# Performance work log

Hardware: AMD Instinct MI355X
Metric: run time of the kernel (lower is better)

## Reference

```python
import jax, jax.numpy as jnp
import numpy as np

SEQ, BS, D, F, E = 1024, 2, 2048, 2048, 8


def setup_inputs() -> dict:
    key = jax.random.key(0)
    ks = jax.random.split(key, 8)
    s = 0.02  # param init scale
    return {
        "hidden_states": jax.random.normal(ks[0], (SEQ, BS, D), jnp.float32),
        "router_w": jax.random.normal(ks[1], (D, E), jnp.float32) * s,
        "gate_w": jax.random.normal(ks[2], (E, D, F), jnp.float32) * s,
        "up_w": jax.random.normal(ks[3], (E, D, F), jnp.float32) * s,
        "down_w": jax.random.normal(ks[4], (E, F, D), jnp.float32) * s,
        "shared_gate_w": jax.random.normal(ks[5], (D, F), jnp.float32) * s,
        "shared_up_w": jax.random.normal(ks[6], (D, F), jnp.float32) * s,
        "shared_down_w": jax.random.normal(ks[7], (F, D), jnp.float32) * s,
    }


def reference(hidden_states, router_w, gate_w, up_w, down_w,
              shared_gate_w, shared_up_w, shared_down_w):
    S, B, Dm = hidden_states.shape
    x = hidden_states.reshape(-1, Dm)          # [T, D] flattened tokens
    # --- router: top-1 expert, sigmoid gate applied to the selected logit ---
    logits = x @ router_w                      # [T, E]
    expert_idx = jnp.argmax(logits, axis=-1)   # top-1 index, [T]
    score = jax.nn.sigmoid(jnp.max(logits, axis=-1))  # [T]
    xs = x * score[:, None]                    # scale BEFORE expert (Llama4)
    # --- per-expert SwiGLU MLP on masked token sets, scatter-combined ---
    n_experts = router_w.shape[1]
    out = jnp.zeros_like(x)
    for e in range(n_experts):                 # small structural loop over experts
        m = (expert_idx == e)[:, None]
        xe = jnp.where(m, xs, 0.0)             # zeroed dispatch (equiv to gather)
        h = jax.nn.silu(xe @ gate_w[e]) * (xe @ up_w[e])
        out = out + jnp.where(m, h @ down_w[e], 0.0)
    # --- shared expert on all tokens ---
    shared = (jax.nn.silu(x @ shared_gate_w) * (x @ shared_up_w)) @ shared_down_w
    return (out + shared).reshape(S, B, Dm)
```

## Files before the change

### kernel.cpp

```cpp
#include <hip/hip_runtime.h>
#include <stdint.h>
#include <math.h>

#define T_TOK 2048
#define DIM   2048
#define FDIM  2048
#define NE    8

#define BM 128
#define BN 128
#define BK 32
#define LDB 40

typedef unsigned short u16;
typedef short s16x8 __attribute__((ext_vector_type(8)));
typedef float f32x4 __attribute__((ext_vector_type(4)));

__device__ __forceinline__ u16 f2bf(float f) {
    union { float f; unsigned int u; } v; v.f = f;
    unsigned int r = v.u + 0x7FFFu + ((v.u >> 16) & 1u);
    return (u16)(r >> 16);
}

__global__ __launch_bounds__(256) void router_k(
    const float* __restrict__ x, const float* __restrict__ rw,
    float* __restrict__ score, int* __restrict__ eidx, int* __restrict__ counts)
{
    int t = blockIdx.x;
    int tid = threadIdx.x;
    float p[8] = {0.f,0.f,0.f,0.f,0.f,0.f,0.f,0.f};
    const float* xrow = x + (size_t)t * DIM;
    for (int d = tid; d < DIM; d += 256) {
        float xv = xrow[d];
        const float4* r = (const float4*)(rw + (size_t)d * 8);
        float4 r0 = r[0], r1 = r[1];
        p[0] += xv * r0.x; p[1] += xv * r0.y; p[2] += xv * r0.z; p[3] += xv * r0.w;
        p[4] += xv * r1.x; p[5] += xv * r1.y; p[6] += xv * r1.z; p[7] += xv * r1.w;
    }
    #pragma unroll
    for (int off = 32; off > 0; off >>= 1) {
        #pragma unroll
        for (int e = 0; e < 8; ++e) p[e] += __shfl_down(p[e], off);
    }
    __shared__ float red[4][8];
    int wave = tid >> 6, lane = tid & 63;
    if (lane == 0) {
        #pragma unroll
        for (int e = 0; e < 8; ++e) red[wave][e] = p[e];
    }
    __syncthreads();
    if (tid == 0) {
        float lg[8];
        #pragma unroll
        for (int e = 0; e < 8; ++e) lg[e] = red[0][e] + red[1][e] + red[2][e] + red[3][e];
        int best = 0; float bv = lg[0];
        #pragma unroll
        for (int e = 1; e < 8; ++e) { if (lg[e] > bv) { bv = lg[e]; best = e; } }
        score[t] = 1.f / (1.f + expf(-bv));
        eidx[t] = best;
        atomicAdd(&counts[best], 1);
    }
}

__global__ void scan_k(const int* __restrict__ counts, int* __restrict__ offs,
                       int* __restrict__ fill)
{
    if (threadIdx.x == 0 && blockIdx.x == 0) {
        int run = 0;
        for (int e = 0; e < NE; ++e) { offs[e] = run; fill[e] = run; run += counts[e]; }
    }
}

__global__ __launch_bounds__(256) void gather_k(
    const float* __restrict__ x, const float* __restrict__ score,
    const int* __restrict__ eidx, int* __restrict__ fill,
    int* __restrict__ tokmap, u16* __restrict__ xsc, u16* __restrict__ xbf)
{
    int t = blockIdx.x, tid = threadIdx.x;
    __shared__ int sp;
    if (tid == 0) {
        int e = eidx[t];
        int p = atomicAdd(&fill[e], 1);
        tokmap[p] = t;
        sp = p;
    }
    __syncthreads();
    int pos = sp;
    float s = score[t];
    const float4* xr = (const float4*)(x + (size_t)t * DIM);
    float4 a = xr[tid * 2], b = xr[tid * 2 + 1];
    alignas(16) u16 raw[8] = { f2bf(a.x), f2bf(a.y), f2bf(a.z), f2bf(a.w),
                               f2bf(b.x), f2bf(b.y), f2bf(b.z), f2bf(b.w) };
    alignas(16) u16 scl[8] = { f2bf(a.x*s), f2bf(a.y*s), f2bf(a.z*s), f2bf(a.w*s),
                               f2bf(b.x*s), f2bf(b.y*s), f2bf(b.z*s), f2bf(b.w*s) };
    *(s16x8*)(xbf + (size_t)t * DIM + tid * 8)   = *(s16x8*)raw;
    *(s16x8*)(xsc + (size_t)pos * DIM + tid * 8) = *(s16x8*)scl;
}

__device__ __forceinline__ void stageB(const float* __restrict__ W, u16* Bs,
                                       int bn, int bkh)
{
    const float* wp = W + (size_t)bkh * FDIM + bn;
    alignas(16) u16 tmp[16];
    #pragma unroll
    for (int j = 0; j < 16; ++j) tmp[j] = f2bf(wp[(size_t)j * FDIM]);
    *(s16x8*)&Bs[bn * LDB + bkh]     = *(s16x8*)&tmp[0];
    *(s16x8*)&Bs[bn * LDB + bkh + 8] = *(s16x8*)&tmp[8];
}

__global__ __launch_bounds__(256) void gateup_k(
    const u16* __restrict__ xsc, const u16* __restrict__ xbf,
    const float* __restrict__ gate_w, const float* __restrict__ up_w,
    const float* __restrict__ sgw, const float* __restrict__ suw,
    const int* __restrict__ counts, const int* __restrict__ offs,
    u16* __restrict__ Hbf, u16* __restrict__ Hs)
{
    int bid = blockIdx.x;
    int g  = bid >> 8;
    int mt = (bid >> 4) & 15;
    int nt = bid & 15;

    int M; const u16* A; const float* Wg; const float* Wu; u16* Ho;
    if (g < NE) {
        M = counts[g];
        int ro = offs[g];
        A  = xsc + (size_t)ro * DIM;
        Wg = gate_w + (size_t)g * DIM * FDIM;
        Wu = up_w  + (size_t)g * DIM * FDIM;
        Ho = Hbf + (size_t)ro * FDIM;
    } else {
        M = T_TOK; A = xbf; Wg = sgw; Wu = suw; Ho = Hs;
    }
    int m0 = mt * BM;
    if (m0 >= M) return;
    int n0 = nt * BN;

    __shared__ u16 As[BM * BK];
    __shared__ u16 Bg[BN * LDB];
    __shared__ u16 Bu[BN * LDB];

    int tid  = threadIdx.x;
    int lane = tid & 63;
    int wave = tid >> 6;
    int wm = (wave >> 1) * 64;
    int wn = (wave & 1) * 64;

    f32x4 accg[4][4], accu[4][4];
    #pragma unroll
    for (int i = 0; i < 4; ++i)
        #pragma unroll
        for (int j = 0; j < 4; ++j) { accg[i][j] = (f32x4)0.f; accu[i][j] = (f32x4)0.f; }

    int ar = tid >> 2;
    int ac = (tid & 3) * 8;
    int arow0 = min(m0 + ar,      M - 1);
    int arow1 = min(m0 + 64 + ar, M - 1);

    int bn  = tid & 127;
    int bkh = (tid >> 7) * 16;

    int am   = wm + (lane & 15);
    int koff = (lane >> 4) * 8;

    for (int k0 = 0; k0 < DIM; k0 += BK) {
        *(s16x8*)&As[ar * BK + ac]        = *(const s16x8*)&A[(size_t)arow0 * DIM + k0 + ac];
        *(s16x8*)&As[(64 + ar) * BK + ac] = *(const s16x8*)&A[(size_t)arow1 * DIM + k0 + ac];
        stageB(Wg + (size_t)k0 * FDIM + n0, Bg, bn, bkh);
        stageB(Wu + (size_t)k0 * FDIM + n0, Bu, bn, bkh);
        __syncthreads();

        s16x8 af[4];
        #pragma unroll
        for (int i = 0; i < 4; ++i)
            af[i] = *(const s16x8*)&As[(am + i * 16) * BK + koff];
        #pragma unroll
        for (int j = 0; j < 4; ++j) {
            int bc = wn + j * 16 + (lane & 15);
            s16x8 bg = *(const s16x8*)&Bg[bc * LDB + koff];
            s16x8 bu = *(const s16x8*)&Bu[bc * LDB + koff];
            #pragma unroll
            for (int i = 0; i < 4; ++i) {
                accg[i][j] = __builtin_amdgcn_mfma_f32_16x16x32_bf16(af[i], bg, accg[i][j], 0, 0, 0);
                accu[i][j] = __builtin_amdgcn_mfma_f32_16x16x32_bf16(af[i], bu, accu[i][j], 0, 0, 0);
            }
        }
        __syncthreads();
    }

    int rbase = wm + ((lane >> 4) << 2);
    int cbase = n0 + wn + (lane & 15);
    #pragma unroll
    for (int i = 0; i < 4; ++i) {
        #pragma unroll
        for (int j = 0; j < 4; ++j) {
            #pragma unroll
            for (int r = 0; r < 4; ++r) {
                int row = m0 + rbase + i * 16 + r;
                if (row < M) {
                    float gv = accg[i][j][r];
                    float uv = accu[i][j][r];
                    float h = gv / (1.f + expf(-gv)) * uv;
                    Ho[(size_t)row * FDIM + cbase + j * 16] = f2bf(h);
                }
            }
        }
    }
}

__global__ __launch_bounds__(256) void down_k(
    const u16* __restrict__ Hbf, const u16* __restrict__ Hs,
    const float* __restrict__ down_w, const float* __restrict__ sdw,
    const int* __restrict__ counts, const int* __restrict__ offs,
    const int* __restrict__ tokmap, float* __restrict__ out)
{
    int bid = blockIdx.x;
    int g  = bid >> 8;
    int mt = (bid >> 4) & 15;
    int nt = bid & 15;

    int M, ro; const u16* A; const float* W;
    if (g < NE) {
        M = counts[g];
        ro = offs[g];
        A = Hbf + (size_t)ro * FDIM;
        W = down_w + (size_t)g * FDIM * DIM;
    } else {
        M = T_TOK; ro = 0; A = Hs; W = sdw;
    }
    int m0 = mt * BM;
    if (m0 >= M) return;
    int n0 = nt * BN;

    __shared__ u16 As[BM * BK];
    __shared__ u16 Bd[BN * LDB];

    int tid  = threadIdx.x;
    int lane = tid & 63;
    int wave = tid >> 6;
    int wm = (wave >> 1) * 64;
    int wn = (wave & 1) * 64;

    f32x4 acc[4][4];
    #pragma unroll
    for (int i = 0; i < 4; ++i)
        #pragma unroll
        for (int j = 0; j < 4; ++j) acc[i][j] = (f32x4)0.f;

    int ar = tid >> 2;
    int ac = (tid & 3) * 8;
    int arow0 = min(m0 + ar,      M - 1);
    int arow1 = min(m0 + 64 + ar, M - 1);
    int bn  = tid & 127;
    int bkh = (tid >> 7) * 16;

    int am   = wm + (lane & 15);
    int koff = (lane >> 4) * 8;

    for (int k0 = 0; k0 < FDIM; k0 += BK) {
        *(s16x8*)&As[ar * BK + ac]        = *(const s16x8*)&A[(size_t)arow0 * FDIM + k0 + ac];
        *(s16x8*)&As[(64 + ar) * BK + ac] = *(const s16x8*)&A[(size_t)arow1 * FDIM + k0 + ac];
        stageB(W + (size_t)k0 * DIM + n0, Bd, bn, bkh);
        __syncthreads();

        s16x8 af[4];
        #pragma unroll
        for (int i = 0; i < 4; ++i)
            af[i] = *(const s16x8*)&As[(am + i * 16) * BK + koff];
        #pragma unroll
        for (int j = 0; j < 4; ++j) {
            int bc = wn + j * 16 + (lane & 15);
            s16x8 bd = *(const s16x8*)&Bd[bc * LDB + koff];
            #pragma unroll
            for (int i = 0; i < 4; ++i)
                acc[i][j] = __builtin_amdgcn_mfma_f32_16x16x32_bf16(af[i], bd, acc[i][j], 0, 0, 0);
        }
        __syncthreads();
    }

    int rbase = wm + ((lane >> 4) << 2);
    int cbase = n0 + wn + (lane & 15);
    #pragma unroll
    for (int i = 0; i < 4; ++i) {
        #pragma unroll
        for (int r = 0; r < 4; ++r) {
            int row = m0 + rbase + i * 16 + r;
            if (row < M) {
                int tok = (g < NE) ? tokmap[ro + row] : row;
                #pragma unroll
                for (int j = 0; j < 4; ++j)
                    atomicAdd(&out[(size_t)tok * DIM + cbase + j * 16], acc[i][j][r]);
            }
        }
    }
}

extern "C" void kernel_launch(void* const* d_in, const int* in_sizes, int n_in,
                              void* d_out, int out_size, void* d_ws, size_t ws_size,
                              hipStream_t stream) {
    const float* x   = (const float*)d_in[0];
    const float* rw  = (const float*)d_in[1];
    const float* gw  = (const float*)d_in[2];
    const float* uw  = (const float*)d_in[3];
    const float* dw  = (const float*)d_in[4];
    const float* sgw = (const float*)d_in[5];
    const float* suw = (const float*)d_in[6];
    const float* sdw = (const float*)d_in[7];
    float* out = (float*)d_out;

    char* ws = (char*)d_ws;
    float* score = (float*)(ws);
    int* eidx    = (int*)(ws + 8192);
    int* counts  = (int*)(ws + 16384);
    int* fill    = (int*)(ws + 16448);
    int* offs    = (int*)(ws + 16512);
    int* tokmap  = (int*)(ws + 16576);
    u16* xsc = (u16*)(ws + 32768);
    u16* xbf = (u16*)(ws + 32768 + 1ull * 8388608);
    u16* Hbf = (u16*)(ws + 32768 + 2ull * 8388608);
    u16* Hs  = (u16*)(ws + 32768 + 3ull * 8388608);

    hipMemsetAsync(counts, 0, 128, stream);
    hipMemsetAsync(out, 0, (size_t)out_size * sizeof(float), stream);

    router_k<<<T_TOK, 256, 0, stream>>>(x, rw, score, eidx, counts);
    scan_k<<<1, 64, 0, stream>>>(counts, offs, fill);
    gather_k<<<T_TOK, 256, 0, stream>>>(x, score, eidx, fill, tokmap, xsc, xbf);
    gateup_k<<<NE * 256 + 256, 256, 0, stream>>>(xsc, xbf, gw, uw, sgw, suw,
                                                 counts, offs, Hbf, Hs);
    down_k<<<NE * 256 + 256, 256, 0, stream>>>(Hbf, Hs, dw, sdw,
                                               counts, offs, tokmap, out);
}
```

Before: 792.1 us.

## Pre-convert weights to transposed bf16 and stage tiles with direct-to-LDS loads

Adds a kernel that converts all expert and shared weights from fp32 to bf16 and transposes them into K-contiguous rows in a workspace buffer each call. The GEMM kernels then load A and B tiles straight into LDS with global_load_lds 16-byte loads, in place of strided fp32 loads plus register conversion. Atomic adds in the down projection become plain stores: expert rows scatter to out and shared-expert rows go to a temp buffer that a final add kernel sums. The trade is a full pass over all 27 weight matrices every call, plus more workspace and launches, and the old path stays as a fallback when the workspace is too small.

```diff
diff --git a/kernel.cpp b/kernel.cpp
--- a/kernel.cpp
+++ b/kernel.cpp
@@ -11,6 +11,7 @@
 #define BN 128
 #define BK 32
 #define LDB 40
+#define MATSZ 4194304ull
 
 typedef unsigned short u16;
 typedef short s16x8 __attribute__((ext_vector_type(8)));
@@ -20,6 +21,11 @@
     union { float f; unsigned int u; } v; v.f = f;
     unsigned int r = v.u + 0x7FFFu + ((v.u >> 16) & 1u);
     return (u16)(r >> 16);
+}
+
+__device__ __forceinline__ void gload_lds16(const void* g, void* l) {
+    __builtin_amdgcn_global_load_lds((const __attribute__((address_space(1))) void*)g,
+                                     (__attribute__((address_space(3))) void*)l, 16, 0, 0);
 }
 
 __global__ __launch_bounds__(256) void router_k(
@@ -97,21 +103,43 @@
     *(s16x8*)(xsc + (size_t)pos * DIM + tid * 8) = *(s16x8*)scl;
 }
 
-__device__ __forceinline__ void stageB(const float* __restrict__ W, u16* Bs,
-                                       int bn, int bkh)
-{
-    const float* wp = W + (size_t)bkh * FDIM + bn;
-    alignas(16) u16 tmp[16];
-    #pragma unroll
-    for (int j = 0; j < 16; ++j) tmp[j] = f2bf(wp[(size_t)j * FDIM]);
-    *(s16x8*)&Bs[bn * LDB + bkh]     = *(s16x8*)&tmp[0];
-    *(s16x8*)&Bs[bn * LDB + bkh + 8] = *(s16x8*)&tmp[8];
+__global__ __launch_bounds__(256) void wtrans_k(
+    const float* __restrict__ gw, const float* __restrict__ uw,
+    const float* __restrict__ dwn, const float* __restrict__ sgw,
+    const float* __restrict__ suw, const float* __restrict__ sdw,
+    u16* __restrict__ wt)
+{
+    int bid = blockIdx.x;
+    int m = bid >> 5;
+    int strip = bid & 31;
+    const float* src;
+    if      (m < 8)  src = gw  + (size_t)m * MATSZ;
+    else if (m < 16) src = uw  + (size_t)(m - 8) * MATSZ;
+    else if (m < 24) src = dwn + (size_t)(m - 16) * MATSZ;
+    else if (m == 24) src = sgw;
+    else if (m == 25) src = suw;
+    else              src = sdw;
+    u16* dst = wt + (size_t)m * MATSZ;
+
+    int tid = threadIdx.x;
+    int n = strip * 64 + (tid & 63);
+    int w = tid >> 6;
+    const float* sp = src + n;
+    u16* dp = dst + (size_t)n * 2048 + w * 512;
+
+    #pragma unroll 2
+    for (int c = 0; c < 64; ++c) {
+        int k = w * 512 + c * 8;
+        alignas(16) u16 t8[8];
+        #pragma unroll
+        for (int j = 0; j < 8; ++j) t8[j] = f2bf(sp[(size_t)(k + j) * 2048]);
+        *(s16x8*)(dp + c * 8) = *(s16x8*)t8;
+    }
 }
 
 __global__ __launch_bounds__(256) void gateup_k(
     const u16* __restrict__ xsc, const u16* __restrict__ xbf,
-    const float* __restrict__ gate_w, const float* __restrict__ up_w,
-    const float* __restrict__ sgw, const float* __restrict__ suw,
+    const u16* __restrict__ wt,
     const int* __restrict__ counts, const int* __restrict__ offs,
     u16* __restrict__ Hbf, u16* __restrict__ Hs)
 {
@@ -120,30 +148,33 @@
     int mt = (bid >> 4) & 15;
     int nt = bid & 15;
 
-    int M; const u16* A; const float* Wg; const float* Wu; u16* Ho;
+    int M; const u16* A; const u16* Wg; const u16* Wu; u16* Ho;
     if (g < NE) {
         M = counts[g];
         int ro = offs[g];
         A  = xsc + (size_t)ro * DIM;
-        Wg = gate_w + (size_t)g * DIM * FDIM;
-        Wu = up_w  + (size_t)g * DIM * FDIM;
+        Wg = wt + (size_t)g * MATSZ;
+        Wu = wt + (size_t)(8 + g) * MATSZ;
         Ho = Hbf + (size_t)ro * FDIM;
     } else {
-        M = T_TOK; A = xbf; Wg = sgw; Wu = suw; Ho = Hs;
+        M = T_TOK; A = xbf;
+        Wg = wt + 24 * MATSZ;
+        Wu = wt + 25 * MATSZ;
+        Ho = Hs;
     }
     int m0 = mt * BM;
     if (m0 >= M) return;
     int n0 = nt * BN;
 
-    __shared__ u16 As[BM * BK];
-    __shared__ u16 Bg[BN * LDB];
-    __shared__ u16 Bu[BN * LDB];
+    __shared__ __align__(128) u16 As[BM * BK];
+    __shared__ __align__(128) u16 Bg[BN * BK];
+    __shared__ __align__(128) u16 Bu[BN * BK];
 
     int tid  = threadIdx.x;
     int lane = tid & 63;
-    int wave = tid >> 6;
-    int wm = (wave >> 1) * 64;
-    int wn = (wave & 1) * 64;
+    int w    = tid >> 6;
+    int wm = (w >> 1) * 64;
+    int wn = (w & 1) * 64;
 
     f32x4 accg[4][4], accu[4][4];
     #pragma unroll
@@ -151,22 +182,29 @@
         #pragma unroll
         for (int j = 0; j < 4; ++j) { accg[i][j] = (f32x4)0.f; accu[i][j] = (f32x4)0.f; }
 
-    int ar = tid >> 2;
-    int ac = (tid & 3) * 8;
-    int arow0 = min(m0 + ar,      M - 1);
-    int arow1 = min(m0 + 64 + ar, M - 1);
-
-    int bn  = tid & 127;
-    int bkh = (tid >> 7) * 16;
+    int r0 = w * 16 + (lane >> 2);
+    int co = (lane & 3) * 8;
+    const u16* gA0  = A  + (size_t)min(m0 + r0,      M - 1) * DIM + co;
+    const u16* gA1  = A  + (size_t)min(m0 + 64 + r0, M - 1) * DIM + co;
+    const u16* gBg0 = Wg + (size_t)(n0 + r0)      * DIM + co;
+    const u16* gBg1 = Wg + (size_t)(n0 + 64 + r0) * DIM + co;
+    const u16* gBu0 = Wu + (size_t)(n0 + r0)      * DIM + co;
+    const u16* gBu1 = Wu + (size_t)(n0 + 64 + r0) * DIM + co;
+    u16* lA0  = As + (w * 16) * BK;
+    u16* lA1  = As + (64 + w * 16) * BK;
+    u16* lBg0 = Bg + (w * 16) * BK;
+    u16* lBg1 = Bg + (64 + w * 16) * BK;
+    u16* lBu0 = Bu + (w * 16) * BK;
+    u16* lBu1 = Bu + (64 + w * 16) * BK;
 
     int am   = wm + (lane & 15);
     int koff = (lane >> 4) * 8;
 
     for (int k0 = 0; k0 < DIM; k0 += BK) {
-        *(s16x8*)&As[ar * BK + ac]        = *(const s16x8*)&A[(size_t)arow0 * DIM + k0 + ac];
-        *(s16x8*)&As[(64 + ar) * BK + ac] = *(const s16x8*)&A[(size_t)arow1 * DIM + k0 + ac];
-        stageB(Wg + (size_t)k0 * FDIM + n0, Bg, bn, bkh);
-        stageB(Wu + (size_t)k0 * FDIM + n0, Bu, bn, bkh);
+        gload_lds16(gA0,  lA0);  gload_lds16(gA1,  lA1);
+        gload_lds16(gBg0, lBg0); gload_lds16(gBg1, lBg1);
+        gload_lds16(gBu0, lBu0); gload_lds16(gBu1, lBu1);
+        gA0 += BK; gA1 += BK; gBg0 += BK; gBg1 += BK; gBu0 += BK; gBu1 += BK;
         __syncthreads();
 
         s16x8 af[4];
@@ -176,8 +214,8 @@
         #pragma unroll
         for (int j = 0; j < 4; ++j) {
             int bc = wn + j * 16 + (lane & 15);
-            s16x8 bg = *(const s16x8*)&Bg[bc * LDB + koff];
-            s16x8 bu = *(const s16x8*)&Bu[bc * LDB + koff];
+            s16x8 bg = *(const s16x8*)&Bg[bc * BK + koff];
+            s16x8 bu = *(const s16x8*)&Bu[bc * BK + koff];
             #pragma unroll
             for (int i = 0; i < 4; ++i) {
                 accg[i][j] = __builtin_amdgcn_mfma_f32_16x16x32_bf16(af[i], bg, accg[i][j], 0, 0, 0);
@@ -209,15 +247,217 @@
 
 __global__ __launch_bounds__(256) void down_k(
     const u16* __restrict__ Hbf, const u16* __restrict__ Hs,
-    const float* __restrict__ down_w, const float* __restrict__ sdw,
+    const u16* __restrict__ wt,
     const int* __restrict__ counts, const int* __restrict__ offs,
-    const int* __restrict__ tokmap, float* __restrict__ out)
+    const int* __restrict__ tokmap, float* __restrict__ out, float* __restrict__ tmpS)
 {
     int bid = blockIdx.x;
     int g  = bid >> 8;
     int mt = (bid >> 4) & 15;
     int nt = bid & 15;
 
+    int M, ro; const u16* A; const u16* W;
+    if (g < NE) {
+        M = counts[g];
+        ro = offs[g];
+        A = Hbf + (size_t)ro * FDIM;
+        W = wt + (size_t)(16 + g) * MATSZ;
+    } else {
+        M = T_TOK; ro = 0; A = Hs; W = wt + 26 * MATSZ;
+    }
+    int m0 = mt * BM;
+    if (m0 >= M) return;
+    int n0 = nt * BN;
+
+    __shared__ __align__(128) u16 As[BM * BK];
+    __shared__ __align__(128) u16 Bd[BN * BK];
+
+    int tid  = threadIdx.x;
+    int lane = tid & 63;
+    int w    = tid >> 6;
+    int wm = (w >> 1) * 64;
+    int wn = (w & 1) * 64;
+
+    f32x4 acc[4][4];
+    #pragma unroll
+    for (int i = 0; i < 4; ++i)
+        #pragma unroll
+        for (int j = 0; j < 4; ++j) acc[i][j] = (f32x4)0.f;
+
+    int r0 = w * 16 + (lane >> 2);
+    int co = (lane & 3) * 8;
+    const u16* gA0 = A + (size_t)min(m0 + r0,      M - 1) * FDIM + co;
+    const u16* gA1 = A + (size_t)min(m0 + 64 + r0, M - 1) * FDIM + co;
+    const u16* gB0 = W + (size_t)(n0 + r0)      * FDIM + co;
+    const u16* gB1 = W + (size_t)(n0 + 64 + r0) * FDIM + co;
+    u16* lA0 = As + (w * 16) * BK;
+    u16* lA1 = As + (64 + w * 16) * BK;
+    u16* lB0 = Bd + (w * 16) * BK;
+    u16* lB1 = Bd + (64 + w * 16) * BK;
+
+    int am   = wm + (lane & 15);
+    int koff = (lane >> 4) * 8;
+
+    for (int k0 = 0; k0 < FDIM; k0 += BK) {
+        gload_lds16(gA0, lA0); gload_lds16(gA1, lA1);
+        gload_lds16(gB0, lB0); gload_lds16(gB1, lB1);
+        gA0 += BK; gA1 += BK; gB0 += BK; gB1 += BK;
+        __syncthreads();
+
+        s16x8 af[4];
+        #pragma unroll
+        for (int i = 0; i < 4; ++i)
+            af[i] = *(const s16x8*)&As[(am + i * 16) * BK + koff];
+        #pragma unroll
+        for (int j = 0; j < 4; ++j) {
+            int bc = wn + j * 16 + (lane & 15);
+            s16x8 bd = *(const s16x8*)&Bd[bc * BK + koff];
+            #pragma unroll
+            for (int i = 0; i < 4; ++i)
+                acc[i][j] = __builtin_amdgcn_mfma_f32_16x16x32_bf16(af[i], bd, acc[i][j], 0, 0, 0);
+        }
+        __syncthreads();
+    }
+
+    int rbase = wm + ((lane >> 4) << 2);
+    int cbase = n0 + wn + (lane & 15);
+    #pragma unroll
+    for (int i = 0; i < 4; ++i) {
+        #pragma unroll
+        for (int r = 0; r < 4; ++r) {
+            int row = m0 + rbase + i * 16 + r;
+            if (row < M) {
+                float* dst;
+                if (g < NE) dst = out + (size_t)tokmap[ro + row] * DIM;
+                else        dst = tmpS + (size_t)row * DIM;
+                #pragma unroll
+                for (int j = 0; j < 4; ++j)
+                    dst[cbase + j * 16] = acc[i][j][r];
+            }
+        }
+    }
+}
+
+__global__ __launch_bounds__(256) void add_k(float* __restrict__ out,
+                                             const float* __restrict__ tmpS)
+{
+    int i = blockIdx.x * 256 + threadIdx.x;
+    float4 o = ((const float4*)out)[i];
+    float4 t = ((const float4*)tmpS)[i];
+    o.x += t.x; o.y += t.y; o.z += t.z; o.w += t.w;
+    ((float4*)out)[i] = o;
+}
+
+__device__ __forceinline__ void stageB_fb(const float* __restrict__ W, u16* Bs,
+                                          int bn, int bkh)
+{
+    const float* wp = W + (size_t)bkh * FDIM + bn;
+    alignas(16) u16 tmp[16];
+    #pragma unroll
+    for (int j = 0; j < 16; ++j) tmp[j] = f2bf(wp[(size_t)j * FDIM]);
+    *(s16x8*)&Bs[bn * LDB + bkh]     = *(s16x8*)&tmp[0];
+    *(s16x8*)&Bs[bn * LDB + bkh + 8] = *(s16x8*)&tmp[8];
+}
+
+__global__ __launch_bounds__(256) void gateup_fb(
+    const u16* __restrict__ xsc, const u16* __restrict__ xbf,
+    const float* __restrict__ gate_w, const float* __restrict__ up_w,
+    const float* __restrict__ sgw, const float* __restrict__ suw,
+    const int* __restrict__ counts, const int* __restrict__ offs,
+    u16* __restrict__ Hbf, u16* __restrict__ Hs)
+{
+    int bid = blockIdx.x;
+    int g  = bid >> 8;
+    int mt = (bid >> 4) & 15;
+    int nt = bid & 15;
+    int M; const u16* A; const float* Wg; const float* Wu; u16* Ho;
+    if (g < NE) {
+        M = counts[g];
+        int ro = offs[g];
+        A  = xsc + (size_t)ro * DIM;
+        Wg = gate_w + (size_t)g * DIM * FDIM;
+        Wu = up_w  + (size_t)g * DIM * FDIM;
+        Ho = Hbf + (size_t)ro * FDIM;
+    } else {
+        M = T_TOK; A = xbf; Wg = sgw; Wu = suw; Ho = Hs;
+    }
+    int m0 = mt * BM;
+    if (m0 >= M) return;
+    int n0 = nt * BN;
+    __shared__ u16 As[BM * BK];
+    __shared__ u16 Bg[BN * LDB];
+    __shared__ u16 Bu[BN * LDB];
+    int tid  = threadIdx.x;
+    int lane = tid & 63;
+    int wave = tid >> 6;
+    int wm = (wave >> 1) * 64;
+    int wn = (wave & 1) * 64;
+    f32x4 accg[4][4], accu[4][4];
+    #pragma unroll
+    for (int i = 0; i < 4; ++i)
+        #pragma unroll
+        for (int j = 0; j < 4; ++j) { accg[i][j] = (f32x4)0.f; accu[i][j] = (f32x4)0.f; }
+    int ar = tid >> 2;
+    int ac = (tid & 3) * 8;
+    int arow0 = min(m0 + ar,      M - 1);
+    int arow1 = min(m0 + 64 + ar, M - 1);
+    int bn  = tid & 127;
+    int bkh = (tid >> 7) * 16;
+    int am   = wm + (lane & 15);
+    int koff = (lane >> 4) * 8;
+    for (int k0 = 0; k0 < DIM; k0 += BK) {
+        *(s16x8*)&As[ar * BK + ac]        = *(const s16x8*)&A[(size_t)arow0 * DIM + k0 + ac];
+        *(s16x8*)&As[(64 + ar) * BK + ac] = *(const s16x8*)&A[(size_t)arow1 * DIM + k0 + ac];
+        stageB_fb(Wg + (size_t)k0 * FDIM + n0, Bg, bn, bkh);
+        stageB_fb(Wu + (size_t)k0 * FDIM + n0, Bu, bn, bkh);
+        __syncthreads();
+        s16x8 af[4];
+        #pragma unroll
+        for (int i = 0; i < 4; ++i)
+            af[i] = *(const s16x8*)&As[(am + i * 16) * BK + koff];
+        #pragma unroll
+        for (int j = 0; j < 4; ++j) {
+            int bc = wn + j * 16 + (lane & 15);
+            s16x8 bg = *(const s16x8*)&Bg[bc * LDB + koff];
+            s16x8 bu = *(const s16x8*)&Bu[bc * LDB + koff];
+            #pragma unroll
+            for (int i = 0; i < 4; ++i) {
+                accg[i][j] = __builtin_amdgcn_mfma_f32_16x16x32_bf16(af[i], bg, accg[i][j], 0, 0, 0);
+                accu[i][j] = __builtin_amdgcn_mfma_f32_16x16x32_bf16(af[i], bu, accu[i][j], 0, 0, 0);
+            }
+        }
+        __syncthreads();
+    }
+    int rbase = wm + ((lane >> 4) << 2);
+    int cbase = n0 + wn + (lane & 15);
+    #pragma unroll
+    for (int i = 0; i < 4; ++i) {
+        #pragma unroll
+        for (int j = 0; j < 4; ++j) {
+            #pragma unroll
+            for (int r = 0; r < 4; ++r) {
+                int row = m0 + rbase + i * 16 + r;
+                if (row < M) {
+                    float gv = accg[i][j][r];
+                    float uv = accu[i][j][r];
+                    float h = gv / (1.f + expf(-gv)) * uv;
+                    Ho[(size_t)row * FDIM + cbase + j * 16] = f2bf(h);
+                }
+            }
+        }
+    }
+}
+
+__global__ __launch_bounds__(256) void down_fb(
+    const u16* __restrict__ Hbf, const u16* __restrict__ Hs,
+    const float* __restrict__ down_w, const float* __restrict__ sdw,
+    const int* __restrict__ counts, const int* __restrict__ offs,
+    const int* __restrict__ tokmap, float* __restrict__ out)
+{
+    int bid = blockIdx.x;
+    int g  = bid >> 8;
+    int mt = (bid >> 4) & 15;
+    int nt = bid & 15;
     int M, ro; const u16* A; const float* W;
     if (g < NE) {
         M = counts[g];
@@ -230,38 +470,31 @@
     int m0 = mt * BM;
     if (m0 >= M) return;
     int n0 = nt * BN;
-
     __shared__ u16 As[BM * BK];
     __shared__ u16 Bd[BN * LDB];
-
     int tid  = threadIdx.x;
     int lane = tid & 63;
     int wave = tid >> 6;
     int wm = (wave >> 1) * 64;
     int wn = (wave & 1) * 64;
-
     f32x4 acc[4][4];
     #pragma unroll
     for (int i = 0; i < 4; ++i)
         #pragma unroll
         for (int j = 0; j < 4; ++j) acc[i][j] = (f32x4)0.f;
-
     int ar = tid >> 2;
     int ac = (tid & 3) * 8;
     int arow0 = min(m0 + ar,      M - 1);
     int arow1 = min(m0 + 64 + ar, M - 1);
     int bn  = tid & 127;
     int bkh = (tid >> 7) * 16;
-
     int am   = wm + (lane & 15);
     int koff = (lane >> 4) * 8;
-
     for (int k0 = 0; k0 < FDIM; k0 += BK) {
         *(s16x8*)&As[ar * BK + ac]        = *(const s16x8*)&A[(size_t)arow0 * FDIM + k0 + ac];
         *(s16x8*)&As[(64 + ar) * BK + ac] = *(const s16x8*)&A[(size_t)arow1 * FDIM + k0 + ac];
-        stageB(W + (size_t)k0 * DIM + n0, Bd, bn, bkh);
-        __syncthreads();
-
+        stageB_fb(W + (size_t)k0 * DIM + n0, Bd, bn, bkh);
+        __syncthreads();
         s16x8 af[4];
         #pragma unroll
         for (int i = 0; i < 4; ++i)
@@ -276,7 +509,6 @@
         }
         __syncthreads();
     }
-
     int rbase = wm + ((lane >> 4) << 2);
     int cbase = n0 + wn + (lane & 15);
     #pragma unroll
@@ -301,7 +533,7 @@
     const float* rw  = (const float*)d_in[1];
     const float* gw  = (const float*)d_in[2];
     const float* uw  = (const float*)d_in[3];
-    const float* dw  = (const float*)d_in[4];
+    const float* dwn = (const float*)d_in[4];
     const float* sgw = (const float*)d_in[5];
     const float* suw = (const float*)d_in[6];
     const float* sdw = (const float*)d_in[7];
@@ -315,18 +547,29 @@
     int* offs    = (int*)(ws + 16512);
     int* tokmap  = (int*)(ws + 16576);
     u16* xsc = (u16*)(ws + 32768);
-    u16* xbf = (u16*)(ws + 32768 + 1ull * 8388608);
-    u16* Hbf = (u16*)(ws + 32768 + 2ull * 8388608);
-    u16* Hs  = (u16*)(ws + 32768 + 3ull * 8388608);
+    u16* xbf = xsc + MATSZ;
+    u16* Hbf = xbf + MATSZ;
+    u16* Hs  = Hbf + MATSZ;
+    float* tmpS = (float*)(ws + 32768 + 4ull * 8388608);
+    u16* wt = (u16*)(ws + 32768 + 4ull * 8388608 + 16777216);
+    const size_t WS_NEED = 32768 + 4ull * 8388608 + 16777216 + 27ull * 8388608;
+    bool big = ws_size >= WS_NEED;
 
     hipMemsetAsync(counts, 0, 128, stream);
-    hipMemsetAsync(out, 0, (size_t)out_size * sizeof(float), stream);
-
     router_k<<<T_TOK, 256, 0, stream>>>(x, rw, score, eidx, counts);
     scan_k<<<1, 64, 0, stream>>>(counts, offs, fill);
     gather_k<<<T_TOK, 256, 0, stream>>>(x, score, eidx, fill, tokmap, xsc, xbf);
-    gateup_k<<<NE * 256 + 256, 256, 0, stream>>>(xsc, xbf, gw, uw, sgw, suw,
-                                                 counts, offs, Hbf, Hs);
-    down_k<<<NE * 256 + 256, 256, 0, stream>>>(Hbf, Hs, dw, sdw,
-                                               counts, offs, tokmap, out);
-}
+
+    if (big) {
+        wtrans_k<<<27 * 32, 256, 0, stream>>>(gw, uw, dwn, sgw, suw, sdw, wt);
+        gateup_k<<<NE * 256 + 256, 256, 0, stream>>>(xsc, xbf, wt, counts, offs, Hbf, Hs);
+        down_k<<<NE * 256 + 256, 256, 0, stream>>>(Hbf, Hs, wt, counts, offs, tokmap, out, tmpS);
+        add_k<<<(T_TOK * DIM) / (256 * 4), 256, 0, stream>>>(out, tmpS);
+    } else {
+        hipMemsetAsync(out, 0, (size_t)out_size * sizeof(float), stream);
+        gateup_fb<<<NE * 256 + 256, 256, 0, stream>>>(xsc, xbf, gw, uw, sgw, suw,
+                                                      counts, offs, Hbf, Hs);
+        down_fb<<<NE * 256 + 256, 256, 0, stream>>>(Hbf, Hs, dwn, sdw,
+                                                    counts, offs, tokmap, out);
+    }
+}
```

After: 981.3 us. 23.9% more time.
